# Kernel tuning notes

Measured on AMD Instinct MI355X. Metric: run time of the kernel, lower is better.

## Reference

```python
import jax, jax.numpy as jnp
import numpy as np

NUM_CLASSES = 22
H_IMG, W_IMG = 256, 320
VOTE_STEPS = 160          # number of discrete steps each pixel votes along its ray
VOTE_THRESH = 0.5         # inlier threshold used by HoughVoterPyTorch


def setup_inputs() -> dict:
    key = jax.random.key(0)
    ks = jax.random.split(key, 24)
    B = 4
    rn = lambda k, s, sc=1.0: (jax.random.normal(k, s, jnp.float32) * sc)
    inp = {
        'x1': rn(ks[0], (B, 512, 8, 10)),
        'x2': rn(ks[1], (B, 256, 16, 20)),
        'x3': rn(ks[2], (B, 128, 32, 40)),
        'x4': rn(ks[3], (B, 64, 64, 80)),
        'x5': rn(ks[4], (B, 64, 128, 160)),
        'depth': jax.random.uniform(ks[5], (B, 1, H_IMG, W_IMG), jnp.float32, 0.5, 3.0),
    }
    raw = jax.random.uniform(ks[6], (B, NUM_CLASSES, H_IMG, W_IMG), jnp.float32)
    inp['seg'] = jnp.where(raw > 0.97, raw, 0.0)  # sparse per-class responses
    inp['fx'] = jnp.float32(572.4); inp['fy'] = jnp.float32(573.6)
    inp['px'] = jnp.float32(W_IMG / 2); inp['py'] = jnp.float32(H_IMG / 2)
    # ConvTranspose2d weights in torch layout [Cin, Cout, kH, kW]
    inp['w5'] = rn(ks[7], (512, 256, 4, 4), 0.02); inp['b5'] = jnp.zeros((256,), jnp.float32)
    inp['w4'] = rn(ks[8], (512, 128, 4, 4), 0.02); inp['b4'] = jnp.zeros((128,), jnp.float32)
    inp['w3'] = rn(ks[9], (256, 64, 4, 4), 0.03);  inp['b3'] = jnp.zeros((64,), jnp.float32)
    inp['w2'] = rn(ks[10], (128, 64, 4, 4), 0.04); inp['b2'] = jnp.zeros((64,), jnp.float32)
    inp['w1'] = rn(ks[11], (128, 64, 4, 4), 0.04); inp['b1'] = jnp.zeros((64,), jnp.float32)
    inp['wv'] = rn(ks[12], (3 * NUM_CLASSES, 64), 0.1); inp['bv'] = jnp.zeros((3 * NUM_CLASSES,), jnp.float32)
    inp['wc'] = rn(ks[13], (NUM_CLASSES, 64), 0.1);     inp['bc'] = jnp.zeros((NUM_CLASSES,), jnp.float32)
    return inp


def conv_t(x, w, b):
    # torch ConvTranspose2d(k=4, s=2, p=1) == dilated conv with flipped kernel
    k = jnp.flip(w, (2, 3)).transpose(1, 0, 2, 3)  # [Cout, Cin, 4, 4]
    y = jax.lax.conv_general_dilated(x, k, (1, 1), ((2, 2), (2, 2)),
                                     lhs_dilation=(2, 2),
                                     dimension_numbers=('NCHW', 'OIHW', 'NCHW'))
    return y + b[None, :, None, None]


def hough_vote(seg2d, dirs, depth2d, fx, fy, px, py):
    # seg2d: [H,W] fused fg prob; dirs: [H,W,2] (dx,dy); depth2d: [H,W]
    H, W = seg2d.shape
    n = dirs / (jnp.linalg.norm(dirs, axis=-1, keepdims=True) + 1e-6)
    u = n[..., 0].reshape(-1)
    v = n[..., 1].reshape(-1)
    ys, xs = jnp.meshgrid(jnp.arange(H, dtype=jnp.float32),
                          jnp.arange(W, dtype=jnp.float32), indexing='ij')
    xs = xs.reshape(-1); ys = ys.reshape(-1)
    w = (seg2d * (seg2d > VOTE_THRESH)).reshape(-1)  # weighted fg votes

    def step(acc, t):
        xt = jnp.round(xs + t * u).astype(jnp.int32)
        yt = jnp.round(ys + t * v).astype(jnp.int32)
        inb = (xt >= 0) & (xt < W) & (yt >= 0) & (yt < H)
        idx = jnp.clip(yt, 0, H - 1) * W + jnp.clip(xt, 0, W - 1)
        return acc.at[idx].add(jnp.where(inb, w, 0.0)), None

    acc, _ = jax.lax.scan(step, jnp.zeros(H * W, jnp.float32),
                          jnp.arange(1, VOTE_STEPS + 1, dtype=jnp.float32))
    vote_map = acc.reshape(H, W)
    ci = jnp.argmax(acc)
    cy = (ci // W).astype(jnp.float32)
    cx = (ci % W).astype(jnp.float32)
    mask = (seg2d > VOTE_THRESH).astype(jnp.float32)
    tz = jnp.sum(depth2d * mask) / (jnp.sum(mask) + 1e-6)
    tx = (cx - px) * tz / fx
    ty = (cy - py) * tz / fy
    return vote_map, jnp.stack([cx, cy]), jnp.stack([tx, ty, tz])


def reference(x1, x2, x3, x4, x5, depth, seg, fx, fy, px, py,
              w5, b5, w4, b4, w3, b3, w2, b2, w1, b1, wv, bv, wc, bc):
    x = jax.nn.relu(conv_t(x1, w5, b5))
    x = jax.nn.relu(conv_t(jnp.concatenate([x, x2], 1), w4, b4))
    x = jax.nn.relu(conv_t(jnp.concatenate([x, x3], 1), w3, b3))
    x = jax.nn.relu(conv_t(jnp.concatenate([x, x4], 1), w2, b2))
    x = jax.nn.relu(conv_t(jnp.concatenate([x, x5], 1), w1, b1))
    bottom_vertex = jnp.einsum('bchw,oc->bohw', x, wv) + bv[None, :, None, None]
    logits = jnp.einsum('bchw,oc->bohw', x, wc) + bc[None, :, None, None]
    bottom_label = jnp.argmax(logits, axis=1)
    center_dirs = jnp.transpose(bottom_vertex[:, :2], (0, 2, 3, 1))  # [B,H,W,2]
    seg_fused = jnp.clip(jnp.sum(seg, axis=1), 0.0, 1.0)             # [B,H,W]
    vote_maps, centers, translations = jax.vmap(
        hough_vote, in_axes=(0, 0, 0, None, None, None, None)
    )(seg_fused, center_dirs, depth[:, 0], fx, fy, px, py)
    return bottom_vertex, bottom_label, vote_maps, centers, translations
```

## Files before the change

kernel.cpp:

```cpp
#include <hip/hip_runtime.h>
#include <cstdint>
#include <cstddef>

#define H_IMG 256
#define W_IMG 320
#define HW_IMG (H_IMG * W_IMG)
#define NCLS 22
#define VOTE_STEPS 160
#define TW 64
#define TH 64
#define NTX 5
#define NTY 4
#define NTILE (NTX * NTY)
#define NCHUNK 16
#define CHPIX (HW_IMG / NCHUNK)

__global__ void repack_kernel(const float* __restrict__ w, double* __restrict__ wp,
                              int CIN, int COUT) {
    int total = CIN * COUT * 16;
    for (int i = blockIdx.x * blockDim.x + threadIdx.x; i < total;
         i += gridDim.x * blockDim.x) {
        int j = i & 3;
        int co = (i >> 2) % COUT;
        int rest = (i >> 2) / COUT;
        int cin = rest % CIN;
        int pp = rest / CIN;
        int ry = pp >> 1, rx = pp & 1;
        int dy = j >> 1, dx = j & 1;
        int ky = 3 - ry - 2 * dy;
        int kx = 3 - rx - 2 * dx;
        wp[i] = (double)w[((size_t)cin * COUT + co) * 16 + ky * 4 + kx];
    }
}

__global__ void repackR_kernel(const float* __restrict__ w, double* __restrict__ wr,
                               int CIN, int COUT) {
    int NCOG = COUT >> 4;
    int total = CIN * COUT * 16;
    for (int i = blockIdx.x * blockDim.x + threadIdx.x; i < total;
         i += gridDim.x * blockDim.x) {
        int tap = i & 3;
        int co = (i >> 2) & 15;
        int rest = i >> 6;
        int cin = rest % CIN;
        int pc = rest / CIN;
        int cog = pc % NCOG;
        int pp = pc / NCOG;
        int ry = pp >> 1, rx = pp & 1;
        int dy = tap >> 1, dxx = tap & 1;
        int ky = 3 - ry - 2 * dy;
        int kx = 3 - rx - 2 * dxx;
        wr[i] = (double)w[((size_t)cin * COUT + (cog * 16 + co)) * 16 + ky * 4 + kx];
    }
}

__global__ void transpose_d_kernel(const float* __restrict__ w, double* __restrict__ wt,
                                   int O, int K) {
    int i = blockIdx.x * blockDim.x + threadIdx.x;
    if (i < O * K) {
        int o = i / K, k = i - o * K;
        wt[k * O + o] = (double)w[i];
    }
}

template <bool RELU_A, bool ADBL>
__global__ __launch_bounds__(256) void convt_part_kernel(
    const void* __restrict__ inA_, int CA,
    const float* __restrict__ inB, int CB,
    const double* __restrict__ wp,
    double* __restrict__ parts,
    int COUT, int Hin, int Win, int nSplit, int B, int TOT) {
    const int NCO = 16;
    const int CIN = CA + CB;
    const int cog = blockIdx.y >> 2;
    const int pp = blockIdx.y & 3;
    const int ry = pp >> 1, rx = pp & 1;
    const int b = blockIdx.z % B;
    const int sp = blockIdx.z / B;
    const int cinPer = CIN / nSplit;
    const int c0 = sp * cinPer, c1 = c0 + cinPer;
    const int co0 = cog * NCO;
    const int plane = Hin * Win;
    const int Hout = Hin * 2, Wout = Win * 2;
    double* out = parts + (size_t)sp * TOT;

    __shared__ double wl[64 * 64];
    for (int i = threadIdx.x; i < cinPer * 64; i += 256) {
        int ci = i >> 6, k = i & 63;
        wl[i] = wp[(((size_t)pp * CIN + c0 + ci) * COUT + co0) * 4 + k];
    }
    __syncthreads();

    for (int p = blockIdx.x * 256 + threadIdx.x; p < plane; p += gridDim.x * 256) {
        int m = p / Win, n = p - m * Win;
        int iy0 = m + ry - 1, ix0 = n + rx - 1;
        int oy = 2 * m + ry, ox = 2 * n + rx;
        double f00 = (iy0 >= 0 && ix0 >= 0) ? 1.0 : 0.0;
        double f01 = (iy0 >= 0 && ix0 + 1 < Win) ? 1.0 : 0.0;
        double f10 = (iy0 + 1 < Hin && ix0 >= 0) ? 1.0 : 0.0;
        double f11 = (iy0 + 1 < Hin && ix0 + 1 < Win) ? 1.0 : 0.0;
        int cy0 = max(iy0, 0), cy1 = min(iy0 + 1, Hin - 1);
        int cx0 = max(ix0, 0), cx1 = min(ix0 + 1, Win - 1);
        int o00 = cy0 * Win + cx0, o01 = cy0 * Win + cx1;
        int o10 = cy1 * Win + cx0, o11 = cy1 * Win + cx1;

        double acc[16];
#pragma unroll
        for (int k = 0; k < 16; ++k) acc[k] = 0.0;

        int a0 = min(c0, CA), a1 = min(c1, CA);
        for (int c = a0; c < a1; ++c) {
            double x00, x01, x10, x11;
            if (ADBL) {
                const double* s = (const double*)inA_ + ((size_t)b * CA + c) * plane;
                x00 = f00 * s[o00]; x01 = f01 * s[o01];
                x10 = f10 * s[o10]; x11 = f11 * s[o11];
            } else {
                const float* s = (const float*)inA_ + ((size_t)b * CA + c) * plane;
                x00 = f00 * (double)s[o00]; x01 = f01 * (double)s[o01];
                x10 = f10 * (double)s[o10]; x11 = f11 * (double)s[o11];
            }
            if (RELU_A) {
                x00 = fmax(x00, 0.0); x01 = fmax(x01, 0.0);
                x10 = fmax(x10, 0.0); x11 = fmax(x11, 0.0);
            }
            const double2* w2 = (const double2*)&wl[(c - c0) * 64];
#pragma unroll
            for (int k = 0; k < 16; ++k) {
                double2 wa = w2[k * 2], wb = w2[k * 2 + 1];
                acc[k] += x00 * wa.x + x01 * wa.y + x10 * wb.x + x11 * wb.y;
            }
        }
        if (CB > 0 && c1 > CA) {
            int b0 = max(c0, CA) - CA, b1 = c1 - CA;
            const float* srcB = inB + (size_t)b * CB * plane;
            for (int c = b0; c < b1; ++c) {
                const float* s = srcB + (size_t)c * plane;
                double x00 = f00 * (double)s[o00], x01 = f01 * (double)s[o01];
                double x10 = f10 * (double)s[o10], x11 = f11 * (double)s[o11];
                const double2* w2 = (const double2*)&wl[(c + CA - c0) * 64];
#pragma unroll
                for (int k = 0; k < 16; ++k) {
                    double2 wa = w2[k * 2], wb = w2[k * 2 + 1];
                    acc[k] += x00 * wa.x + x01 * wa.y + x10 * wb.x + x11 * wb.y;
                }
            }
        }

        size_t ob = ((size_t)b * COUT + co0) * (size_t)Hout * Wout +
                    (size_t)oy * Wout + ox;
#pragma unroll
        for (int k = 0; k < 16; ++k)
            out[ob + (size_t)k * Hout * Wout] = acc[k];
    }
}

__global__ void reduce_part_kernel(const double* __restrict__ parts,
                                   const float* __restrict__ bias,
                                   double* __restrict__ out,
                                   int nSplit, int COUT, int HWo, int TOT) {
    int i = blockIdx.x * blockDim.x + threadIdx.x;
    if (i < TOT) {
        double a = (double)bias[(i / HWo) % COUT];
        for (int sp = 0; sp < nSplit; ++sp) a += parts[(size_t)sp * TOT + i];
        out[i] = a;
    }
}

template <int PX>
__global__ __launch_bounds__(256) void convt_reg_kernel(
    const double* __restrict__ zin, const float* __restrict__ xin,
    const double* __restrict__ wr,
    const float* __restrict__ bias,
    double* __restrict__ out,
    int COUT, int Hin, int Win) {
    const int NCOG = COUT >> 4;
    const int plane = Hin * Win;
    const int Wq = Win / PX;
    const int cog = blockIdx.y >> 2, pp = blockIdx.y & 3;
    const int ry = pp >> 1, rx = pp & 1;
    const int b = blockIdx.z;
    __shared__ double wl[4096];

    int t = blockIdx.x * 256 + threadIdx.x;
    int m = t / Wq, n0 = (t - m * Wq) * PX;
    int r0 = m + ry - 1, r1 = r0 + 1;
    double mr0 = (r0 >= 0) ? 1.0 : 0.0;
    double mr1 = (r1 < Hin) ? 1.0 : 0.0;
    int cr0 = max(r0, 0) * Win, cr1 = min(r1, Hin - 1) * Win;
    const int ib = rx ? 0 : 1;
    const int eidx = rx ? PX : 0;
    int eoff = rx ? min(n0 + PX, Win - 1) : max(n0 - 1, 0);
    double me = rx ? ((n0 + PX < Win) ? 1.0 : 0.0) : ((n0 > 0) ? 1.0 : 0.0);
    double me0 = me * mr0, me1 = me * mr1;

    double acc[16][PX];
#pragma unroll
    for (int k = 0; k < 16; ++k) {
        double bvv = (double)bias[cog * 16 + k];
#pragma unroll
        for (int tt = 0; tt < PX; ++tt) acc[k][tt] = bvv;
    }

    const double* wbase = wr + (size_t)(pp * NCOG + cog) * 128 * 64;

    for (int i = threadIdx.x; i < 4096; i += 256) wl[i] = wbase[i];
    __syncthreads();
    {
        const double* s = zin + (size_t)b * 64 * plane;
        for (int c = 0; c < 64; ++c) {
            double xa0[PX + 1], xa1[PX + 1];
#pragma unroll
            for (int j = 0; j < PX / 2; ++j) {
                double2 v0 = *(const double2*)(s + cr0 + n0 + 2 * j);
                double2 v1 = *(const double2*)(s + cr1 + n0 + 2 * j);
                xa0[ib + 2 * j] = mr0 * fmax(v0.x, 0.0);
                xa0[ib + 2 * j + 1] = mr0 * fmax(v0.y, 0.0);
                xa1[ib + 2 * j] = mr1 * fmax(v1.x, 0.0);
                xa1[ib + 2 * j + 1] = mr1 * fmax(v1.y, 0.0);
            }
            xa0[eidx] = me0 * fmax(s[cr0 + eoff], 0.0);
            xa1[eidx] = me1 * fmax(s[cr1 + eoff], 0.0);
            const double2* w2 = (const double2*)&wl[c * 64];
#pragma unroll
            for (int co = 0; co < 16; ++co) {
                double2 wa = w2[co * 2], wb = w2[co * 2 + 1];
#pragma unroll
                for (int tt = 0; tt < PX; ++tt)
                    acc[co][tt] += wa.x * xa0[tt] + wa.y * xa0[tt + 1] +
                                   wb.x * xa1[tt] + wb.y * xa1[tt + 1];
            }
            s += plane;
        }
    }
    __syncthreads();
    for (int i = threadIdx.x; i < 4096; i += 256) wl[i] = wbase[4096 + i];
    __syncthreads();
    {
        const float* s = xin + (size_t)b * 64 * plane;
        for (int c = 0; c < 64; ++c) {
            double xa0[PX + 1], xa1[PX + 1];
#pragma unroll
            for (int j = 0; j < PX / 2; ++j) {
                float2 v0 = *(const float2*)(s + cr0 + n0 + 2 * j);
                float2 v1 = *(const float2*)(s + cr1 + n0 + 2 * j);
                xa0[ib + 2 * j] = mr0 * (double)v0.x;
                xa0[ib + 2 * j + 1] = mr0 * (double)v0.y;
                xa1[ib + 2 * j] = mr1 * (double)v1.x;
                xa1[ib + 2 * j + 1] = mr1 * (double)v1.y;
            }
            xa0[eidx] = me0 * (double)s[cr0 + eoff];
            xa1[eidx] = me1 * (double)s[cr1 + eoff];
            const double2* w2 = (const double2*)&wl[c * 64];
#pragma unroll
            for (int co = 0; co < 16; ++co) {
                double2 wa = w2[co * 2], wb = w2[co * 2 + 1];
#pragma unroll
                for (int tt = 0; tt < PX; ++tt)
                    acc[co][tt] += wa.x * xa0[tt] + wa.y * xa0[tt + 1] +
                                   wb.x * xa1[tt] + wb.y * xa1[tt + 1];
            }
            s += plane;
        }
    }

    int oy = 2 * m + ry;
    size_t ob = (size_t)(b * COUT + cog * 16) * plane * 4 + (size_t)oy * (Win * 2);
#pragma unroll
    for (int co = 0; co < 16; ++co)
#pragma unroll
        for (int tt = 0; tt < PX; ++tt)
            out[ob + (size_t)co * plane * 4 + 2 * (n0 + tt) + rx] = acc[co][tt];
}

__global__ __launch_bounds__(256) void head_lds_kernel(
    const double* __restrict__ z5,
    const double* __restrict__ wvT,
    const float* __restrict__ bv,
    const double* __restrict__ wcT,
    const float* __restrict__ bc,
    float* __restrict__ vert, double* __restrict__ dirs,
    float* __restrict__ label) {
    int p = blockIdx.x * 256 + threadIdx.x;
    int half = blockIdx.y;
    int b = blockIdx.z;
    __shared__ double wl[64 * 44];
    if (half == 0) {
        for (int i = threadIdx.x; i < 64 * 44; i += 256) {
            int c = i / 44, k = i - c * 44;
            wl[i] = wvT[c * 66 + k];
        }
    } else {
        for (int i = threadIdx.x; i < 64 * 44; i += 256) {
            int c = i / 44, k = i - c * 44;
            wl[i] = (k < 22) ? wvT[c * 66 + 44 + k] : wcT[c * 22 + (k - 22)];
        }
    }
    __syncthreads();

    const double* xp = z5 + (size_t)b * 64 * HW_IMG + p;
    if (half == 0) {
        double acc[44];
#pragma unroll
        for (int k = 0; k < 44; ++k) acc[k] = (double)bv[k];
        for (int c = 0; c < 64; ++c) {
            double x = fmax(xp[(size_t)c * HW_IMG], 0.0);
            const double2* w2 = (const double2*)&wl[c * 44];
#pragma unroll
            for (int j = 0; j < 22; ++j) {
                double2 w = w2[j];
                acc[2 * j] += x * w.x; acc[2 * j + 1] += x * w.y;
            }
        }
        float* op = vert + (size_t)b * 66 * HW_IMG + p;
#pragma unroll
        for (int k = 0; k < 44; ++k) op[(size_t)k * HW_IMG] = (float)acc[k];
        dirs[(size_t)b * 2 * HW_IMG + p] = acc[0];
        dirs[(size_t)b * 2 * HW_IMG + HW_IMG + p] = acc[1];
    } else {
        double acc[22], lg[22];
#pragma unroll
        for (int k = 0; k < 22; ++k) { acc[k] = (double)bv[44 + k]; lg[k] = (double)bc[k]; }
        for (int c = 0; c < 64; ++c) {
            double x = fmax(xp[(size_t)c * HW_IMG], 0.0);
            const double2* w2 = (const double2*)&wl[c * 44];
#pragma unroll
            for (int j = 0; j < 11; ++j) {
                double2 w = w2[j];
                acc[2 * j] += x * w.x; acc[2 * j + 1] += x * w.y;
            }
#pragma unroll
            for (int j = 0; j < 11; ++j) {
                double2 w = w2[11 + j];
                lg[2 * j] += x * w.x; lg[2 * j + 1] += x * w.y;
            }
        }
        float* op = vert + ((size_t)b * 66 + 44) * HW_IMG + p;
#pragma unroll
        for (int k = 0; k < 22; ++k) op[(size_t)k * HW_IMG] = (float)acc[k];
        int bi = 0; double bvv = lg[0];
#pragma unroll
        for (int k = 1; k < 22; ++k)
            if (lg[k] > bvv) { bvv = lg[k]; bi = k; }
        label[(size_t)b * HW_IMG + p] = (float)bi;
    }
}

__global__ __launch_bounds__(256) void vote_prep_kernel(
    const float* __restrict__ seg, const float* __restrict__ depth,
    const double* __restrict__ dirs,
    double* __restrict__ rayS, double* __restrict__ rayU,
    double* __restrict__ rayV, double* __restrict__ rayRU,
    double* __restrict__ rayRV, double* __restrict__ rayN,
    double* __restrict__ sums) {
    int p = blockIdx.x * 256 + threadIdx.x;
    int b = blockIdx.z;
    double s = 0.0;
    const float* sp = seg + (size_t)b * NCLS * HW_IMG + p;
    for (int c = 0; c < NCLS; ++c) s += (double)sp[(size_t)c * HW_IMG];
    s = fmin(fmax(s, 0.0), 1.0);
    bool msk = s > 0.5;
    double d = (double)depth[(size_t)b * HW_IMG + p];
    double dm = msk ? d : 0.0;
    double mm = msk ? 1.0 : 0.0;
    for (int off = 32; off > 0; off >>= 1) {
        dm += __shfl_down(dm, off);
        mm += __shfl_down(mm, off);
    }
    __shared__ double sdm[4], smm[4];
    int wid = threadIdx.x >> 6, lane = threadIdx.x & 63;
    if (lane == 0) { sdm[wid] = dm; smm[wid] = mm; }
    __syncthreads();
    if (threadIdx.x == 0) {
        atomicAdd(&sums[b * 2 + 0], sdm[0] + sdm[1] + sdm[2] + sdm[3]);
        atomicAdd(&sums[b * 2 + 1], smm[0] + smm[1] + smm[2] + smm[3]);
    }
    size_t idx = (size_t)b * HW_IMG + p;
    if (msk) {
        double dx = dirs[(size_t)b * 2 * HW_IMG + p];
        double dy = dirs[(size_t)b * 2 * HW_IMG + HW_IMG + p];
        double nrm = sqrt(dx * dx + dy * dy) + 1e-6;
        double u = dx / nrm, v = dy / nrm;
        double xf = (double)(p % W_IMG), yf = (double)(p / W_IMG);
        double tmax = 1e30;
        if (u > 1e-9)       tmax = fmin(tmax, ((double)W_IMG - 0.25 - xf) / u);
        else if (u < -1e-9) tmax = fmin(tmax, (-0.75 - xf) / u);
        if (v > 1e-9)       tmax = fmin(tmax, ((double)H_IMG - 0.25 - yf) / v);
        else if (v < -1e-9) tmax = fmin(tmax, (-0.75 - yf) / v);
        int nst = VOTE_STEPS;
        if (tmax < (double)VOTE_STEPS) nst = (int)tmax + 1;
        rayS[idx] = s;
        rayU[idx] = u;
        rayV[idx] = v;
        rayRU[idx] = (u != 0.0) ? 1.0 / u : 0.0;
        rayRV[idx] = (v != 0.0) ? 1.0 / v : 0.0;
        rayN[idx] = (double)nst;
    } else {
        rayS[idx] = 0.0;
    }
}

__global__ __launch_bounds__(256) void vote_tile_kernel(
    const double* __restrict__ rayS, const double* __restrict__ rayU,
    const double* __restrict__ rayV, const double* __restrict__ rayRU,
    const double* __restrict__ rayRV, const double* __restrict__ rayN,
    double* __restrict__ vparts) {
    int chunk = blockIdx.x;
    int tile = blockIdx.y;
    int b = blockIdx.z;
    int tx0 = (tile % NTX) * TW, ty0 = (tile / NTX) * TH;
    __shared__ double vt[TW * TH];
    for (int i = threadIdx.x; i < TW * TH; i += 256) vt[i] = 0.0;
    __syncthreads();

    size_t base = (size_t)b * HW_IMG;
    int p0 = chunk * CHPIX;
    for (int q = threadIdx.x; q < CHPIX; q += 256) {
        int p = p0 + q;
        double s = rayS[base + p];
        if (s == 0.0) continue;
        double u = rayU[base + p], v = rayV[base + p];
        double ru = rayRU[base + p], rv = rayRV[base + p];
        int nst = (int)rayN[base + p];
        double xf = (double)(p % W_IMG), yf = (double)(p / W_IMG);
        double ta = 1.0, tb = (double)nst;
        if (ru != 0.0) {
            double lo = ((double)(tx0 - 1) - xf) * ru;
            double hi = ((double)(tx0 + TW) - xf) * ru;
            ta = fmax(ta, fmin(lo, hi));
            tb = fmin(tb, fmax(lo, hi));
        } else {
            if (xf < (double)(tx0 - 1) || xf > (double)(tx0 + TW)) continue;
        }
        if (rv != 0.0) {
            double lo = ((double)(ty0 - 1) - yf) * rv;
            double hi = ((double)(ty0 + TH) - yf) * rv;
            ta = fmax(ta, fmin(lo, hi));
            tb = fmin(tb, fmax(lo, hi));
        } else {
            if (yf < (double)(ty0 - 1) || yf > (double)(ty0 + TH)) continue;
        }
        if (ta > tb) continue;
        int t0 = (int)ceil(ta), t1 = (int)floor(tb);
        for (int t = t0; t <= t1; ++t) {
            double tf = (double)t;
            int xi = (int)rint(xf + tf * u);
            int yi = (int)rint(yf + tf * v);
            if (xi >= tx0 && xi < tx0 + TW && yi >= ty0 && yi < ty0 + TH)
                atomicAdd(&vt[(yi - ty0) * TW + (xi - tx0)], s);
        }
    }
    __syncthreads();
    double* dst = vparts + (((size_t)chunk * 4 + b) * NTILE + tile) * (TW * TH);
    for (int i = threadIdx.x; i < TW * TH; i += 256) dst[i] = vt[i];
}

__global__ void vote_reduce_kernel(const double* __restrict__ vparts,
                                   double* __restrict__ voteacc,
                                   float* __restrict__ vote) {
    int i = blockIdx.x * 256 + threadIdx.x;
    if (i < 4 * HW_IMG) {
        int b = i / HW_IMG, cell = i - b * HW_IMG;
        int y = cell / W_IMG, x = cell - y * W_IMG;
        int tile = (y / TH) * NTX + (x / TW);
        int ci = (y % TH) * TW + (x % TW);
        double a = 0.0;
        for (int c = 0; c < NCHUNK; ++c)
            a += vparts[(((size_t)c * 4 + b) * NTILE + tile) * (TW * TH) + ci];
        voteacc[i] = a;
        vote[i] = (float)a;
    }
}

__global__ __launch_bounds__(1024) void center_d_kernel(
    const double* __restrict__ voteacc, const double* __restrict__ sums,
    const float* __restrict__ fx, const float* __restrict__ fy,
    const float* __restrict__ px, const float* __restrict__ py,
    float* __restrict__ centers, float* __restrict__ transl) {
    int b = blockIdx.x;
    const double* vb = voteacc + (size_t)b * HW_IMG;
    double best = -1.0;
    int bi = HW_IMG;
    for (int i = threadIdx.x; i < HW_IMG; i += 1024) {
        double v = vb[i];
        if (v > best || (v == best && i < bi)) { best = v; bi = i; }
    }
    for (int off = 32; off > 0; off >>= 1) {
        double ov = __shfl_down(best, off);
        int oi = __shfl_down(bi, off);
        if (ov > best || (ov == best && oi < bi)) { best = ov; bi = oi; }
    }
    __shared__ double sbv[16];
    __shared__ int sbi[16];
    int wid = threadIdx.x >> 6, lane = threadIdx.x & 63;
    if (lane == 0) { sbv[wid] = best; sbi[wid] = bi; }
    __syncthreads();
    if (threadIdx.x == 0) {
        for (int q = 1; q < 16; ++q)
            if (sbv[q] > best || (sbv[q] == best && sbi[q] < bi)) {
                best = sbv[q]; bi = sbi[q];
            }
        double cx = (double)(bi % W_IMG), cy = (double)(bi / W_IMG);
        double tz = sums[b * 2 + 0] / (sums[b * 2 + 1] + 1e-6);
        double tx = (cx - (double)px[0]) * tz / (double)fx[0];
        double ty = (cy - (double)py[0]) * tz / (double)fy[0];
        centers[b * 2 + 0] = (float)cx;
        centers[b * 2 + 1] = (float)cy;
        transl[b * 3 + 0] = (float)tx;
        transl[b * 3 + 1] = (float)ty;
        transl[b * 3 + 2] = (float)tz;
    }
}

extern "C" void kernel_launch(void* const* d_in, const int* in_sizes, int n_in,
                              void* d_out, int out_size, void* d_ws, size_t ws_size,
                              hipStream_t stream) {
    const float* x1 = (const float*)d_in[0];
    const float* x2 = (const float*)d_in[1];
    const float* x3 = (const float*)d_in[2];
    const float* x4 = (const float*)d_in[3];
    const float* x5 = (const float*)d_in[4];
    const float* depth = (const float*)d_in[5];
    const float* seg = (const float*)d_in[6];
    const float* fx = (const float*)d_in[7];
    const float* fy = (const float*)d_in[8];
    const float* px = (const float*)d_in[9];
    const float* py = (const float*)d_in[10];
    const float* w5 = (const float*)d_in[11];
    const float* b5 = (const float*)d_in[12];
    const float* w4 = (const float*)d_in[13];
    const float* b4 = (const float*)d_in[14];
    const float* w3 = (const float*)d_in[15];
    const float* b3 = (const float*)d_in[16];
    const float* w2 = (const float*)d_in[17];
    const float* b2 = (const float*)d_in[18];
    const float* w1 = (const float*)d_in[19];
    const float* b1 = (const float*)d_in[20];
    const float* wv = (const float*)d_in[21];
    const float* bv = (const float*)d_in[22];
    const float* wc = (const float*)d_in[23];
    const float* bc = (const float*)d_in[24];

    float* out = (float*)d_out;
    float* vert = out;
    float* label = vert + (size_t)4 * 66 * HW_IMG;
    float* vote = label + (size_t)4 * HW_IMG;
    float* centers = vote + (size_t)4 * HW_IMG;
    float* transl = centers + 8;

    double* zA = (double*)d_ws;
    double* zB = zA + 20971520;
    double* dirs = zB + 5242880;
    double* voteacc = dirs + 655360;
    double* sums = voteacc + 327680;
    double* wp5 = sums + 8;
    double* wp4 = wp5 + 2097152;
    double* wp3 = wp4 + 1048576;
    double* wr2 = wp3 + 262144;
    double* wr1 = wr2 + 131072;
    double* wvT = wr1 + 131072;
    double* wcT = wvT + 4224;
    double* z1 = zA; double* z2 = zB; double* z3 = zA; double* z4 = zB; double* z5 = zA;
    double* parts = zA + 2000000;
    double* rayS = zB;
    double* rayU = zB + 327680;
    double* rayV = zB + 2 * 327680;
    double* rayRU = zB + 3 * 327680;
    double* rayRV = zB + 4 * 327680;
    double* rayN = zB + 5 * 327680;
    double* vparts = zA;

    hipMemsetAsync(sums, 0, 8 * sizeof(double), stream);

    auto rp = [&](const float* w, double* wp, int CIN, int COUT) {
        int total = CIN * COUT * 16;
        repack_kernel<<<(total + 255) / 256, 256, 0, stream>>>(w, wp, CIN, COUT);
    };
    rp(w5, wp5, 512, 256);
    rp(w4, wp4, 512, 128);
    rp(w3, wp3, 256, 64);
    repackR_kernel<<<(131072 + 255) / 256, 256, 0, stream>>>(w2, wr2, 128, 64);
    repackR_kernel<<<(131072 + 255) / 256, 256, 0, stream>>>(w1, wr1, 128, 64);
    transpose_d_kernel<<<(66 * 64 + 255) / 256, 256, 0, stream>>>(wv, wvT, 66, 64);
    transpose_d_kernel<<<(22 * 64 + 255) / 256, 256, 0, stream>>>(wc, wcT, 22, 64);

    convt_part_kernel<false, false><<<dim3(1, 64, 32), 256, 0, stream>>>(
        x1, 512, nullptr, 0, wp5, parts, 256, 8, 10, 8, 4, 327680);
    reduce_part_kernel<<<1280, 256, 0, stream>>>(parts, b5, z1, 8, 256, 320, 327680);
    convt_part_kernel<true, true><<<dim3(2, 32, 32), 256, 0, stream>>>(
        z1, 256, x2, 256, wp4, parts, 128, 16, 20, 8, 4, 655360);
    reduce_part_kernel<<<2560, 256, 0, stream>>>(parts, b4, z2, 8, 128, 1280, 655360);
    convt_part_kernel<true, true><<<dim3(5, 16, 16), 256, 0, stream>>>(
        z2, 128, x3, 128, wp3, parts, 64, 32, 40, 4, 4, 1310720);
    reduce_part_kernel<<<5120, 256, 0, stream>>>(parts, b3, z3, 4, 64, 5120, 1310720);
    convt_reg_kernel<2><<<dim3(10, 16, 4), 256, 0, stream>>>(
        z3, x4, wr2, b2, z4, 64, 64, 80);
    convt_reg_kernel<2><<<dim3(40, 16, 4), 256, 0, stream>>>(
        z4, x5, wr1, b1, z5, 64, 128, 160);

    head_lds_kernel<<<dim3(320, 2, 4), 256, 0, stream>>>(z5, wvT, bv, wcT, bc,
                                                         vert, dirs, label);

    vote_prep_kernel<<<dim3(320, 1, 4), 256, 0, stream>>>(
        seg, depth, dirs, rayS, rayU, rayV, rayRU, rayRV, rayN, sums);
    vote_tile_kernel<<<dim3(NCHUNK, NTILE, 4), 256, 0, stream>>>(
        rayS, rayU, rayV, rayRU, rayRV, rayN, vparts);
    vote_reduce_kernel<<<(4 * HW_IMG + 255) / 256, 256, 0, stream>>>(
        vparts, voteacc, vote);
    center_d_kernel<<<4, 1024, 0, stream>>>(voteacc, sums, fx, fy, px, py,
                                            centers, transl);
}
```

Before: 1.955 ms.

## Add specialized first-layer convT kernel covering all four parities per block

```diff
diff --git a/kernel.cpp b/kernel.cpp
--- a/kernel.cpp
+++ b/kernel.cpp
@@ -64,7 +64,7 @@
 }
 
 template <bool RELU_A, bool ADBL>
-__global__ __launch_bounds__(256) void convt_part_kernel(
+__global__ __launch_bounds__(320) void convt_part_kernel(
     const void* __restrict__ inA_, int CA,
     const float* __restrict__ inB, int CB,
     const double* __restrict__ wp,
@@ -82,16 +82,17 @@
     const int co0 = cog * NCO;
     const int plane = Hin * Win;
     const int Hout = Hin * 2, Wout = Win * 2;
+    const int bs = blockDim.x;
     double* out = parts + (size_t)sp * TOT;
 
     __shared__ double wl[64 * 64];
-    for (int i = threadIdx.x; i < cinPer * 64; i += 256) {
+    for (int i = threadIdx.x; i < cinPer * 64; i += bs) {
         int ci = i >> 6, k = i & 63;
         wl[i] = wp[(((size_t)pp * CIN + c0 + ci) * COUT + co0) * 4 + k];
     }
     __syncthreads();
 
-    for (int p = blockIdx.x * 256 + threadIdx.x; p < plane; p += gridDim.x * 256) {
+    for (int p = blockIdx.x * bs + threadIdx.x; p < plane; p += gridDim.x * bs) {
         int m = p / Win, n = p - m * Win;
         int iy0 = m + ry - 1, ix0 = n + rx - 1;
         int oy = 2 * m + ry, ox = 2 * n + rx;
@@ -153,6 +154,70 @@
         for (int k = 0; k < 16; ++k)
             out[ob + (size_t)k * Hout * Wout] = acc[k];
     }
+}
+
+__global__ __launch_bounds__(320) void convt_part_l1_kernel(
+    const float* __restrict__ xin, int CIN,
+    const double* __restrict__ wp,
+    double* __restrict__ parts,
+    int COUT, int nSplit, int B, int TOT) {
+    const int Hin = 8, Win = 10, plane = 80;
+    const int Hout = 16, Wout = 20;
+    const int cog = blockIdx.y;
+    const int b = blockIdx.z % B;
+    const int sp = blockIdx.z / B;
+    const int cinPer = CIN / nSplit;
+    const int c0 = sp * cinPer;
+    const int co0 = cog * 16;
+    const int pp = threadIdx.x / plane;
+    const int p = threadIdx.x - pp * plane;
+    const int ry = pp >> 1, rx = pp & 1;
+    double* out = parts + (size_t)sp * TOT;
+
+    __shared__ double wl[4 * 32 * 64];
+    for (int i = threadIdx.x; i < 4 * cinPer * 64; i += 320) {
+        int k = i & 63;
+        int ci = (i >> 6) % cinPer;
+        int pq = (i >> 6) / cinPer;
+        wl[i] = wp[(((size_t)pq * CIN + c0 + ci) * COUT + co0) * 4 + k];
+    }
+    __syncthreads();
+
+    int m = p / Win, n = p - m * Win;
+    int iy0 = m + ry - 1, ix0 = n + rx - 1;
+    int oy = 2 * m + ry, ox = 2 * n + rx;
+    double f00 = (iy0 >= 0 && ix0 >= 0) ? 1.0 : 0.0;
+    double f01 = (iy0 >= 0 && ix0 + 1 < Win) ? 1.0 : 0.0;
+    double f10 = (iy0 + 1 < Hin && ix0 >= 0) ? 1.0 : 0.0;
+    double f11 = (iy0 + 1 < Hin && ix0 + 1 < Win) ? 1.0 : 0.0;
+    int cy0 = max(iy0, 0), cy1 = min(iy0 + 1, Hin - 1);
+    int cx0 = max(ix0, 0), cx1 = min(ix0 + 1, Win - 1);
+    int o00 = cy0 * Win + cx0, o01 = cy0 * Win + cx1;
+    int o10 = cy1 * Win + cx0, o11 = cy1 * Win + cx1;
+
+    double acc[16];
+#pragma unroll
+    for (int k = 0; k < 16; ++k) acc[k] = 0.0;
+
+    const float* s = xin + ((size_t)b * CIN + c0) * plane;
+    const double* wpp = &wl[pp * cinPer * 64];
+    for (int c = 0; c < cinPer; ++c) {
+        double x00 = f00 * (double)s[o00], x01 = f01 * (double)s[o01];
+        double x10 = f10 * (double)s[o10], x11 = f11 * (double)s[o11];
+        const double2* w2 = (const double2*)&wpp[c * 64];
+#pragma unroll
+        for (int k = 0; k < 16; ++k) {
+            double2 wa = w2[k * 2], wb = w2[k * 2 + 1];
+            acc[k] += x00 * wa.x + x01 * wa.y + x10 * wb.x + x11 * wb.y;
+        }
+        s += plane;
+    }
+
+    size_t ob = ((size_t)b * COUT + co0) * (size_t)Hout * Wout +
+                (size_t)oy * Wout + ox;
+#pragma unroll
+    for (int k = 0; k < 16; ++k)
+        out[ob + (size_t)k * Hout * Wout] = acc[k];
 }
 
 __global__ void reduce_part_kernel(const double* __restrict__ parts,
@@ -584,10 +649,10 @@
     transpose_d_kernel<<<(66 * 64 + 255) / 256, 256, 0, stream>>>(wv, wvT, 66, 64);
     transpose_d_kernel<<<(22 * 64 + 255) / 256, 256, 0, stream>>>(wc, wcT, 22, 64);
 
-    convt_part_kernel<false, false><<<dim3(1, 64, 32), 256, 0, stream>>>(
-        x1, 512, nullptr, 0, wp5, parts, 256, 8, 10, 8, 4, 327680);
-    reduce_part_kernel<<<1280, 256, 0, stream>>>(parts, b5, z1, 8, 256, 320, 327680);
-    convt_part_kernel<true, true><<<dim3(2, 32, 32), 256, 0, stream>>>(
+    convt_part_l1_kernel<<<dim3(1, 16, 64), 320, 0, stream>>>(
+        x1, 512, wp5, parts, 256, 16, 4, 327680);
+    reduce_part_kernel<<<1280, 256, 0, stream>>>(parts, b5, z1, 16, 256, 320, 327680);
+    convt_part_kernel<true, true><<<dim3(1, 32, 32), 320, 0, stream>>>(
         z1, 256, x2, 256, wp4, parts, 128, 16, 20, 8, 4, 655360);
     reduce_part_kernel<<<2560, 256, 0, stream>>>(parts, b4, z2, 8, 128, 1280, 655360);
     convt_part_kernel<true, true><<<dim3(5, 16, 16), 256, 0, stream>>>(
```

After: 1.955 ms (median of 2 runs). Within noise of the previous version (-0.0%).
